# Optimization experiments

Hardware: AMD Instinct MI355X
Metric: run time of the kernel (lower is better)

Reference implementation:

```python
import jax, jax.numpy as jnp
import numpy as np

N, D = 4096, 512
TAU, ALPHA, BETA = 0.8, 0.55, 0.4
ADJ_P = 0.005  # sparse binary adjacency density (avg degree ~20)


def setup_inputs() -> dict:
    key = jax.random.key(0)
    ks = jax.random.split(key, 8)
    z1 = jax.random.normal(ks[0], (N, D), dtype=jnp.float32)
    z2 = jax.random.normal(ks[1], (N, D), dtype=jnp.float32)

    def adj(k):
        a = jax.random.bernoulli(k, ADJ_P, (N, N)).astype(jnp.float32)
        # adjacency masks are binary {0,1}; zero the diagonal like the model does
        return a * (1.0 - jnp.eye(N, dtype=jnp.float32))

    return {
        "z1": z1,
        "z2": z2,
        "adj_c": adj(ks[2]),
        "adj_m": adj(ks[3]),
        "adj_f": adj(ks[4]),
        "adj_c_aug": adj(ks[5]),
        "adj_m_aug": adj(ks[6]),
        "adj_f_aug": adj(ks[7]),
    }


def _normalize(z):
    # F.normalize(z, dim=1): divide by L2 norm clamped at 1e-12
    n = jnp.maximum(jnp.linalg.norm(z, axis=1, keepdims=True), 1e-12)
    return z / n


def _cl_loss(z, z_aug, adj, tau):
    zn = _normalize(z)
    zan = _normalize(z_aug)
    intra = jnp.exp((zn @ zn.T) / tau)          # [N, N]
    inter = jnp.exp((zn @ zan.T) / tau)         # [N, N]
    intra_diag = jnp.diagonal(intra)
    positive = jnp.diagonal(inter) + (intra * adj).sum(1) + (inter * adj).sum(1)
    denom = intra.sum(1) + inter.sum(1) - intra_diag
    adj_count = adj.sum(1) * 2.0 + 1.0
    loss = jnp.log(positive / denom) / adj_count
    return -jnp.mean(loss)


def _final_cl_loss(z, z_aug, adj, adj_aug, tau):
    return ALPHA * _cl_loss(z, z_aug, adj, tau) + BETA * _cl_loss(z_aug, z, adj_aug, tau)


def reference(z1, z2, adj_c, adj_m, adj_f, adj_c_aug, adj_m_aug, adj_f_aug):
    loss_coarse = _final_cl_loss(z1, z2, adj_c, adj_c_aug, TAU)
    loss_medium = _final_cl_loss(z1, z2, adj_m, adj_m_aug, TAU)
    loss_fine = _final_cl_loss(z1, z2, adj_f, adj_f_aug, TAU)
    loss_cross_cf = _final_cl_loss(z1, z2, adj_c, adj_f_aug, TAU * 0.8)
    loss_cross_mf = _final_cl_loss(z1, z2, adj_m, adj_f_aug, TAU * 0.9)

    sc, sm, sf = adj_c.sum(), adj_m.sum(), adj_f.sum()
    total_info = sc + sm + sf + 1e-08
    scale_loss = (sc / total_info) * loss_coarse + (sm / total_info) * loss_medium + (sf / total_info) * loss_fine
    cross_loss = 0.2 * (loss_cross_cf + loss_cross_mf)
    return scale_loss + cross_loss
```

## Files before the change

### kernel.cpp

```cpp
#include <hip/hip_runtime.h>
#include <hip/hip_bf16.h>

#define NR 4096
#define DD 512
#define CAP 64

typedef __bf16 bf16x8 __attribute__((ext_vector_type(8)));
typedef float f32x4 __attribute__((ext_vector_type(4)));
typedef unsigned short u16;

#define AS_GLOBAL(p) ((const __attribute__((address_space(1))) unsigned int*)(p))
#define AS_LDS(p)    ((__attribute__((address_space(3))) unsigned int*)(p))

__device__ __forceinline__ u16 f2bf(float x) {
    __hip_bfloat16 h = __float2bfloat16(x);
    return *reinterpret_cast<u16*>(&h);
}

__device__ __forceinline__ float blo(unsigned u) { return __uint_as_float(u << 16); }
__device__ __forceinline__ float bhi(unsigned u) { return __uint_as_float(u & 0xffff0000u); }

__global__ void norm_kernel(const float* z1, const float* z2,
                            u16* zn1, u16* zn2, float* d12) {
    const int row = blockIdx.x;
    const int t = threadIdx.x;
    const float* r1 = z1 + (size_t)row * DD;
    const float* r2 = z2 + (size_t)row * DD;
    float a0 = r1[t], a1 = r1[t + 256];
    float b0 = r2[t], b1 = r2[t + 256];
    float ss1 = a0 * a0 + a1 * a1;
    float ss2 = b0 * b0 + b1 * b1;
    #pragma unroll
    for (int m = 1; m < 64; m <<= 1) {
        ss1 += __shfl_xor(ss1, m);
        ss2 += __shfl_xor(ss2, m);
    }
    __shared__ float s1s[4], s2s[4], ds[4];
    const int wid = t >> 6, lane = t & 63;
    if (lane == 0) { s1s[wid] = ss1; s2s[wid] = ss2; }
    __syncthreads();
    const float n1 = s1s[0] + s1s[1] + s1s[2] + s1s[3];
    const float n2 = s2s[0] + s2s[1] + s2s[2] + s2s[3];
    const float inv1 = 1.0f / fmaxf(sqrtf(n1), 1e-12f);
    const float inv2 = 1.0f / fmaxf(sqrtf(n2), 1e-12f);
    const float u0 = a0 * inv1, u1 = a1 * inv1;
    const float v0 = b0 * inv2, v1 = b1 * inv2;
    zn1[(size_t)row * DD + t]       = f2bf(u0);
    zn1[(size_t)row * DD + t + 256] = f2bf(u1);
    zn2[(size_t)row * DD + t]       = f2bf(v0);
    zn2[(size_t)row * DD + t + 256] = f2bf(v1);
    float dp = u0 * v0 + u1 * v1;
    #pragma unroll
    for (int m = 1; m < 64; m <<= 1) dp += __shfl_xor(dp, m);
    if (lane == 0) ds[wid] = dp;
    __syncthreads();
    if (t == 0) d12[row] = ds[0] + ds[1] + ds[2] + ds[3];
}

__global__ __launch_bounds__(256, 3)
void fused_kernel(const u16* __restrict__ zn1, const u16* __restrict__ zn2,
                  const float* __restrict__ m0, const float* __restrict__ m1,
                  const float* __restrict__ m2, const float* __restrict__ m3,
                  const float* __restrict__ m4, const float* __restrict__ m5,
                  float* __restrict__ part, float* __restrict__ ms,
                  float* __restrict__ asum) {
    __shared__ u16 As[128 * 64];
    __shared__ u16 Bs[128 * 64];

    const int bid = blockIdx.x;
    const int tid = threadIdx.x;
    const int lane = tid & 63;

    const float C0 = 1.8033688011112042f;
    const float C1 = 2.2542110013890054f;
    const float C2 = 2.0037431123457825f;

    const int g5 = bid / 5;
    const int r5 = bid - g5 * 5;

    if (r5 < 2) {
        const int id = g5 * 2 + r5;
        int mode, by, bx;
        if (id < 1024) {
            mode = 1; by = id >> 5; bx = id & 31;
        } else {
            int k = id - 1024;
            mode = 0;
            if (k >= 528) { k -= 528; mode = 2; }
            int v = (int)((65.0f - sqrtf(4225.0f - 8.0f * (float)k)) * 0.5f);
            if (v < 0) v = 0; if (v > 31) v = 31;
            while (v < 31 && (v + 1) * 32 - ((v + 1) * v) / 2 <= k) v++;
            while (v > 0 && v * 32 - (v * (v - 1)) / 2 > k) v--;
            by = v;
            bx = by + (k - (by * 32 - (by * (by - 1)) / 2));
        }
        const int Ib = by * 128, Jb = bx * 128;
        const u16* Ag = (mode == 2) ? zn2 : zn1;
        const u16* Bg = (mode == 0) ? zn1 : zn2;
        const int p_row = mode;
        const int p_col = (mode == 1) ? 3 : mode;
        const bool do_cols = (mode == 1) || (bx != by);

        const int wid = tid >> 6;
        const int wm = wid >> 1, wn = wid & 1;
        const int quad = lane >> 4, lcol = lane & 15;

        f32x4 acc[4][4];
        #pragma unroll
        for (int a = 0; a < 4; a++)
            #pragma unroll
            for (int b = 0; b < 4; b++)
                acc[a][b] = (f32x4){0.f, 0.f, 0.f, 0.f};

        unsigned oA[4], oB[4];
        #pragma unroll
        for (int cc = 0; cc < 4; cc++) {
            const int ch = cc * 4 + wid;
            const int p = ch * 64 + lane;
            const int r = p >> 3;
            const int kb = (p & 7) ^ (r & 7);
            oA[cc] = (unsigned)((Ib + r) * DD + kb * 8);
            oB[cc] = (unsigned)((Jb + r) * DD + kb * 8);
        }

        for (int k0 = 0; k0 < DD; k0 += 64) {
            __syncthreads();
            #pragma unroll
            for (int cc = 0; cc < 4; cc++) {
                const unsigned lo = (unsigned)(cc * 4 + wid) * 1024u;
                __builtin_amdgcn_global_load_lds(AS_GLOBAL(Ag + oA[cc] + k0),
                                                 AS_LDS((char*)As + lo), 16, 0, 0);
                __builtin_amdgcn_global_load_lds(AS_GLOBAL(Bg + oB[cc] + k0),
                                                 AS_LDS((char*)Bs + lo), 16, 0, 0);
            }
            __syncthreads();
            #pragma unroll
            for (int kk = 0; kk < 64; kk += 32) {
                const int kbb = (kk >> 3) + quad;
                bf16x8 a[4], b[4];
                #pragma unroll
                for (int i = 0; i < 4; i++) {
                    const int ra = wm * 64 + i * 16 + lcol;
                    const int rb = wn * 64 + i * 16 + lcol;
                    a[i] = *(const bf16x8*)&As[ra * 64 + ((kbb ^ (ra & 7)) * 8)];
                    b[i] = *(const bf16x8*)&Bs[rb * 64 + ((kbb ^ (rb & 7)) * 8)];
                }
                #pragma unroll
                for (int mi = 0; mi < 4; mi++)
                    #pragma unroll
                    for (int ni = 0; ni < 4; ni++)
                        acc[mi][ni] = __builtin_amdgcn_mfma_f32_16x16x32_bf16(a[mi], b[ni], acc[mi][ni], 0, 0, 0);
            }
        }

        __syncthreads();
        float* eb = (float*)As;
        float* sRow = eb;
        float* sCol = eb + 768;

        float colacc[3][4];
        #pragma unroll
        for (int t = 0; t < 3; t++)
            #pragma unroll
            for (int ni = 0; ni < 4; ni++) colacc[t][ni] = 0.f;

        #pragma unroll
        for (int mi = 0; mi < 4; mi++) {
            #pragma unroll
            for (int reg = 0; reg < 4; reg++) {
                float p0 = 0.f, p1 = 0.f, p2 = 0.f;
                #pragma unroll
                for (int ni = 0; ni < 4; ni++) {
                    const float s = acc[mi][ni][reg];
                    const float e0 = __builtin_amdgcn_exp2f(s * C0);
                    const float e1 = __builtin_amdgcn_exp2f(s * C1);
                    const float e2 = __builtin_amdgcn_exp2f(s * C2);
                    p0 += e0; p1 += e1; p2 += e2;
                    colacc[0][ni] += e0; colacc[1][ni] += e1; colacc[2][ni] += e2;
                }
                #pragma unroll
                for (int msk = 1; msk < 16; msk <<= 1) {
                    p0 += __shfl_xor(p0, msk);
                    p1 += __shfl_xor(p1, msk);
                    p2 += __shfl_xor(p2, msk);
                }
                if (lcol == 0) {
                    const int r = wm * 64 + mi * 16 + quad * 4 + reg;
                    sRow[wn * 384 + 0 * 128 + r] = p0;
                    sRow[wn * 384 + 1 * 128 + r] = p1;
                    sRow[wn * 384 + 2 * 128 + r] = p2;
                }
            }
        }
        #pragma unroll
        for (int t = 0; t < 3; t++) {
            #pragma unroll
            for (int ni = 0; ni < 4; ni++) {
                float v = colacc[t][ni];
                v += __shfl_xor(v, 16); v += __shfl_xor(v, 32);
                if (quad == 0) sCol[wm * 384 + t * 128 + wn * 64 + ni * 16 + lcol] = v;
            }
        }
        __syncthreads();
        if (tid < 128) {
            const int i = Ib + tid;
            #pragma unroll
            for (int t = 0; t < 3; t++) {
                const float v = sRow[t * 128 + tid] + sRow[384 + t * 128 + tid];
                part[(((size_t)p_row * 3 + t) * 32 + bx) * NR + i] = v;
            }
        } else if (do_cols) {
            const int c = tid - 128;
            const int j = Jb + c;
            #pragma unroll
            for (int t = 0; t < 3; t++) {
                const float v = sCol[t * 128 + c] + sCol[384 + t * 128 + c];
                part[(((size_t)p_col * 3 + t) * 32 + by) * NR + j] = v;
            }
        }
    } else {
        const int sid = g5 * 3 + (r5 - 2);
        if (sid >= 3072) return;
        const int widx = tid >> 6;
        const int grp = lane >> 4;
        const int l = lane & 15;
        const int wbase = sid * 8 + widx * 2;
        const int m = wbase >> 12;
        const int i0 = wbase & (NR - 1);

        const float* M = (m == 0) ? m0 : (m == 1) ? m1 : (m == 2) ? m2
                       : (m == 3) ? m3 : (m == 4) ? m4 : m5;
        const float4* p0 = (const float4*)(M + (size_t)i0 * NR) + lane;
        const float4* p1 = (const float4*)(M + (size_t)(i0 + 1) * NR) + lane;
        unsigned long long mask0 = 0ull, mask1 = 0ull;
        #pragma unroll
        for (int t = 0; t < 16; t++) {
            const float4 va = p0[t * 64];
            const float4 vb = p1[t * 64];
            mask0 |= (unsigned long long)((va.x != 0.f ? 1u : 0u)
                   | (va.y != 0.f ? 2u : 0u)
                   | (va.z != 0.f ? 4u : 0u)
                   | (va.w != 0.f ? 8u : 0u)) << (t * 4);
            mask1 |= (unsigned long long)((vb.x != 0.f ? 1u : 0u)
                   | (vb.y != 0.f ? 2u : 0u)
                   | (vb.z != 0.f ? 4u : 0u)
                   | (vb.w != 0.f ? 8u : 0u)) << (t * 4);
        }
        const int n0 = __popcll(mask0), n1 = __popcll(mask1);
        int off0 = n0, off1 = n1;
        #pragma unroll
        for (int d = 1; d < 64; d <<= 1) {
            const int t0 = __shfl_up(off0, d);
            const int t1 = __shfl_up(off1, d);
            if (lane >= d) { off0 += t0; off1 += t1; }
        }
        const int total0 = __shfl(off0, 63), total1 = __shfl(off1, 63);
        int* lidx0 = ((int*)As) + widx * 128;
        int* lidx1 = lidx0 + 64;
        int pos = off0 - n0;
        unsigned long long mm = mask0;
        while (mm) {
            const int b = __ffsll(mm) - 1;
            mm &= mm - 1;
            if (pos < CAP) lidx0[pos] = ((b >> 2) * 64 + lane) * 4 + (b & 3);
            pos++;
        }
        pos = off1 - n1;
        mm = mask1;
        while (mm) {
            const int b = __ffsll(mm) - 1;
            mm &= mm - 1;
            if (pos < CAP) lidx1[pos] = ((b >> 2) * 64 + lane) * 4 + (b & 3);
            pos++;
        }
        if (lane == 63) {
            asum[(size_t)m * NR + i0]     = (float)total0;
            asum[(size_t)m * NR + i0 + 1] = (float)total1;
        }
        const int cnt0 = min(total0, CAP), cnt1 = min(total1, CAP);
        const int jreg0 = lidx0[lane];
        const int jreg1 = lidx1[lane];

        int nslot; int slot[3]; float coef[3];
        switch (m) {
            case 0: nslot = 2; slot[0] = 0; coef[0] = C0; slot[1] = 3; coef[1] = C1; break;
            case 1: nslot = 2; slot[0] = 1; coef[0] = C0; slot[1] = 4; coef[1] = C2; break;
            case 2: nslot = 1; slot[0] = 2; coef[0] = C0; break;
            case 3: nslot = 1; slot[0] = 0; coef[0] = C0; break;
            case 4: nslot = 1; slot[0] = 1; coef[0] = C0; break;
            default: nslot = 3; slot[0] = 2; coef[0] = C0; slot[1] = 3; coef[1] = C1;
                     slot[2] = 4; coef[2] = C2; break;
        }

        const u16* A = (m < 3) ? zn1 : zn2;

        for (int rr = 0; rr < 2; rr++) {
            const int i = i0 + rr;
            const int cnt = rr ? cnt1 : cnt0;
            const int jreg = rr ? jreg1 : jreg0;

            unsigned au[16];
            {
                const uint4* ap = (const uint4*)(A + (size_t)i * DD) + l * 4;
                #pragma unroll
                for (int t = 0; t < 4; t++) {
                    const uint4 r = ap[t];
                    au[t * 4 + 0] = r.x; au[t * 4 + 1] = r.y;
                    au[t * 4 + 2] = r.z; au[t * 4 + 3] = r.w;
                }
            }

            float acc[3][2] = {{0.f, 0.f}, {0.f, 0.f}, {0.f, 0.f}};

            for (int q0 = 0; q0 < cnt; q0 += 4) {
                const int q = q0 + grp;
                const bool valid = q < cnt;
                const int j = __shfl(jreg, valid ? q : 0);

                const uint4* pj1 = (const uint4*)(zn1 + (size_t)j * DD) + l * 4;
                const uint4* pj2 = (const uint4*)(zn2 + (size_t)j * DD) + l * 4;
                uint4 r1[4], r2[4];
                #pragma unroll
                for (int t = 0; t < 4; t++) { r1[t] = pj1[t]; r2[t] = pj2[t]; }

                float s10 = 0.f, s11 = 0.f, s20 = 0.f, s21 = 0.f;
                #pragma unroll
                for (int t = 0; t < 4; t++) {
                    const unsigned* u1 = (const unsigned*)&r1[t];
                    const unsigned* u2 = (const unsigned*)&r2[t];
                    #pragma unroll
                    for (int qd = 0; qd < 4; qd++) {
                        const unsigned aw = au[t * 4 + qd];
                        const float alo = blo(aw), ahi = bhi(aw);
                        s10 += alo * blo(u1[qd]); s11 += ahi * bhi(u1[qd]);
                        s20 += alo * blo(u2[qd]); s21 += ahi * bhi(u2[qd]);
                    }
                }
                float d1 = s10 + s11, d2 = s20 + s21;
                #pragma unroll
                for (int msk = 1; msk < 16; msk <<= 1) {
                    d1 += __shfl_xor(d1, msk);
                    d2 += __shfl_xor(d2, msk);
                }
                const float e1 = (m < 3) ? d1 : d2;
                const float e2 = (m < 3) ? d2 : d1;
                if (valid) {
                    for (int s = 0; s < nslot; s++) {
                        acc[s][0] += __builtin_amdgcn_exp2f(e1 * coef[s]);
                        acc[s][1] += __builtin_amdgcn_exp2f(e2 * coef[s]);
                    }
                }
            }

            #pragma unroll
            for (int s = 0; s < 3; s++) {
                #pragma unroll
                for (int h = 0; h < 2; h++) {
                    float v = acc[s][h];
                    v += __shfl_xor(v, 16);
                    v += __shfl_xor(v, 32);
                    acc[s][h] = v;
                }
            }
            if (lane == 0) {
                const int pb = (m < 3) ? 0 : 2;
                for (int s = 0; s < nslot; s++) {
                    ms[((pb)     * 5 + slot[s]) * NR + i] = acc[s][0];
                    ms[((pb + 1) * 5 + slot[s]) * NR + i] = acc[s][1];
                }
            }
        }
    }
}

__global__ __launch_bounds__(256)
void reduce_kernel(const float* __restrict__ part, float* __restrict__ rs) {
    const int g = blockIdx.x * 256 + threadIdx.x;
    const int pt = g >> 12;
    const int i = g & (NR - 1);
    const float* base = part + ((size_t)pt * 32) * NR + i;
    float s = 0.f;
    #pragma unroll
    for (int k = 0; k < 32; k++) s += base[(size_t)k * NR];
    rs[(size_t)pt * NR + i] = s;
}

__global__ void finalize_kernel(const float* rs, const float* ms, const float* asum,
                                const float* d12, float* out) {
    const int t = threadIdx.x;
    const int tA[5] = {0, 0, 0, 1, 2};
    const int kA[5] = {0, 1, 2, 3, 4};
    const int aA[5] = {0, 1, 2, 0, 1};
    const int aB[5] = {3, 4, 5, 5, 5};
    const float it[3] = {1.25f, 1.5625f, 1.3888888888888888f};
    const float e1t[3] = {expf(1.25f), expf(1.5625f), expf(1.3888888888888888f)};

    float LA[5] = {0, 0, 0, 0, 0}, LB[5] = {0, 0, 0, 0, 0};
    float sc = 0.f, sm = 0.f, sf = 0.f;

    for (int i = t; i < NR; i += 256) {
        const float d = d12[i];
        float ed[3];
        ed[0] = __expf(d * it[0]); ed[1] = __expf(d * it[1]); ed[2] = __expf(d * it[2]);
        float R[4][3], M[4][5], A6[6];
        #pragma unroll
        for (int p = 0; p < 4; p++) {
            #pragma unroll
            for (int tt = 0; tt < 3; tt++) R[p][tt] = rs[(p * 3 + tt) * NR + i];
            #pragma unroll
            for (int k = 0; k < 5; k++) M[p][k] = ms[(p * 5 + k) * NR + i];
        }
        #pragma unroll
        for (int a = 0; a < 6; a++) A6[a] = asum[a * NR + i];

        #pragma unroll
        for (int c = 0; c < 5; c++) {
            const int tt = tA[c], k = kA[c];
            float pos = ed[tt] + M[0][k] + M[1][k];
            float den = R[0][tt] + R[1][tt] - e1t[tt];
            float cnt = 2.f * A6[aA[c]] + 1.f;
            LA[c] += __logf(pos / den) / cnt;
            pos = ed[tt] + M[2][k] + M[3][k];
            den = R[2][tt] + R[3][tt] - e1t[tt];
            cnt = 2.f * A6[aB[c]] + 1.f;
            LB[c] += __logf(pos / den) / cnt;
        }
        sc += A6[0]; sm += A6[1]; sf += A6[2];
    }

    __shared__ float red[256];
    float vals[13] = {LA[0], LA[1], LA[2], LA[3], LA[4],
                      LB[0], LB[1], LB[2], LB[3], LB[4], sc, sm, sf};
    __shared__ float tot[13];
    for (int q = 0; q < 13; q++) {
        red[t] = vals[q];
        __syncthreads();
        for (int s = 128; s > 0; s >>= 1) {
            if (t < s) red[t] += red[t + s];
            __syncthreads();
        }
        if (t == 0) tot[q] = red[0];
        __syncthreads();
    }
    if (t == 0) {
        float Ac[5], Bc[5];
        #pragma unroll
        for (int c = 0; c < 5; c++) {
            Ac[c] = -tot[c] / (float)NR;
            Bc[c] = -tot[5 + c] / (float)NR;
        }
        const float ALPHA = 0.55f, BETA = 0.4f;
        const float Lc  = ALPHA * Ac[0] + BETA * Bc[0];
        const float Lm  = ALPHA * Ac[1] + BETA * Bc[1];
        const float Lf  = ALPHA * Ac[2] + BETA * Bc[2];
        const float Lcf = ALPHA * Ac[3] + BETA * Bc[3];
        const float Lmf = ALPHA * Ac[4] + BETA * Bc[4];
        const float scs = tot[10], sms = tot[11], sfs = tot[12];
        const float tot_info = scs + sms + sfs + 1e-8f;
        out[0] = (scs * Lc + sms * Lm + sfs * Lf) / tot_info + 0.2f * (Lcf + Lmf);
    }
}

extern "C" void kernel_launch(void* const* d_in, const int* in_sizes, int n_in,
                              void* d_out, int out_size, void* d_ws, size_t ws_size,
                              hipStream_t stream) {
    const float* z1  = (const float*)d_in[0];
    const float* z2  = (const float*)d_in[1];
    const float* ac  = (const float*)d_in[2];
    const float* am  = (const float*)d_in[3];
    const float* af  = (const float*)d_in[4];
    const float* aca = (const float*)d_in[5];
    const float* ama = (const float*)d_in[6];
    const float* afa = (const float*)d_in[7];

    float* ws   = (float*)d_ws;
    float* rs   = ws;
    float* ms   = rs + 12 * NR;
    float* asum = ms + 20 * NR;
    float* d12  = asum + 6 * NR;
    u16* zn1 = (u16*)(d12 + NR);
    u16* zn2 = zn1 + (size_t)NR * DD;
    float* part = (float*)(zn2 + (size_t)NR * DD);

    norm_kernel<<<NR, 256, 0, stream>>>(z1, z2, zn1, zn2, d12);
    fused_kernel<<<5200, 256, 0, stream>>>(zn1, zn2, ac, am, af, aca, ama, afa,
                                           part, ms, asum);
    reduce_kernel<<<12 * NR / 256, 256, 0, stream>>>(part, rs);
    finalize_kernel<<<1, 256, 0, stream>>>(rs, ms, asum, d12, (float*)d_out);
}
```

Baseline: 511.7 us.

## Use 512-thread blocks with 8 waves per 128x128 similarity tile

Doubles the fused kernel's block size from 256 to 512 threads. Each 128x128 GEMM tile is now split across 8 waves in a 2x4 grid, each owning a 64x32 sub-tile, and each adjacency-mask block processes 16 rows instead of 8. The interleaving of GEMM and mask blocks and the grid size are rebalanced to match. The aim is more waves per tile and fewer accumulator registers per wave, for better latency hiding. The cost is more LDS reads per MFMA, since A fragments are reloaded by more waves, plus an extra partial-sum reduction step in the epilogue.

```diff
diff --git a/kernel.cpp b/kernel.cpp
--- a/kernel.cpp
+++ b/kernel.cpp
@@ -57,7 +57,7 @@
     if (t == 0) d12[row] = ds[0] + ds[1] + ds[2] + ds[3];
 }
 
-__global__ __launch_bounds__(256, 3)
+__global__ __launch_bounds__(512, 3)
 void fused_kernel(const u16* __restrict__ zn1, const u16* __restrict__ zn2,
                   const float* __restrict__ m0, const float* __restrict__ m1,
                   const float* __restrict__ m2, const float* __restrict__ m3,
@@ -75,11 +75,11 @@
     const float C1 = 2.2542110013890054f;
     const float C2 = 2.0037431123457825f;
 
-    const int g5 = bid / 5;
-    const int r5 = bid - g5 * 5;
-
-    if (r5 < 2) {
-        const int id = g5 * 2 + r5;
+    const int g7 = bid / 7;
+    const int r7 = bid - g7 * 7;
+
+    if (r7 < 4) {
+        const int id = g7 * 4 + r7;
         int mode, by, bx;
         if (id < 1024) {
             mode = 1; by = id >> 5; bx = id & 31;
@@ -102,20 +102,21 @@
         const bool do_cols = (mode == 1) || (bx != by);
 
         const int wid = tid >> 6;
-        const int wm = wid >> 1, wn = wid & 1;
+        const int wm = wid >> 2;
+        const int wn = wid & 3;
         const int quad = lane >> 4, lcol = lane & 15;
 
-        f32x4 acc[4][4];
+        f32x4 acc[4][2];
         #pragma unroll
         for (int a = 0; a < 4; a++)
             #pragma unroll
-            for (int b = 0; b < 4; b++)
+            for (int b = 0; b < 2; b++)
                 acc[a][b] = (f32x4){0.f, 0.f, 0.f, 0.f};
 
-        unsigned oA[4], oB[4];
-        #pragma unroll
-        for (int cc = 0; cc < 4; cc++) {
-            const int ch = cc * 4 + wid;
+        unsigned oA[2], oB[2];
+        #pragma unroll
+        for (int cc = 0; cc < 2; cc++) {
+            const int ch = cc * 8 + wid;
             const int p = ch * 64 + lane;
             const int r = p >> 3;
             const int kb = (p & 7) ^ (r & 7);
@@ -126,8 +127,8 @@
         for (int k0 = 0; k0 < DD; k0 += 64) {
             __syncthreads();
             #pragma unroll
-            for (int cc = 0; cc < 4; cc++) {
-                const unsigned lo = (unsigned)(cc * 4 + wid) * 1024u;
+            for (int cc = 0; cc < 2; cc++) {
+                const unsigned lo = (unsigned)(cc * 8 + wid) * 1024u;
                 __builtin_amdgcn_global_load_lds(AS_GLOBAL(Ag + oA[cc] + k0),
                                                  AS_LDS((char*)As + lo), 16, 0, 0);
                 __builtin_amdgcn_global_load_lds(AS_GLOBAL(Bg + oB[cc] + k0),
@@ -137,18 +138,21 @@
             #pragma unroll
             for (int kk = 0; kk < 64; kk += 32) {
                 const int kbb = (kk >> 3) + quad;
-                bf16x8 a[4], b[4];
+                bf16x8 a[4], b[2];
                 #pragma unroll
                 for (int i = 0; i < 4; i++) {
                     const int ra = wm * 64 + i * 16 + lcol;
-                    const int rb = wn * 64 + i * 16 + lcol;
                     a[i] = *(const bf16x8*)&As[ra * 64 + ((kbb ^ (ra & 7)) * 8)];
+                }
+                #pragma unroll
+                for (int i = 0; i < 2; i++) {
+                    const int rb = wn * 32 + i * 16 + lcol;
                     b[i] = *(const bf16x8*)&Bs[rb * 64 + ((kbb ^ (rb & 7)) * 8)];
                 }
                 #pragma unroll
                 for (int mi = 0; mi < 4; mi++)
                     #pragma unroll
-                    for (int ni = 0; ni < 4; ni++)
+                    for (int ni = 0; ni < 2; ni++)
                         acc[mi][ni] = __builtin_amdgcn_mfma_f32_16x16x32_bf16(a[mi], b[ni], acc[mi][ni], 0, 0, 0);
             }
         }
@@ -156,13 +160,13 @@
         __syncthreads();
         float* eb = (float*)As;
         float* sRow = eb;
-        float* sCol = eb + 768;
-
-        float colacc[3][4];
+        float* sCol = eb + 1536;
+
+        float colacc[3][2];
         #pragma unroll
         for (int t = 0; t < 3; t++)
             #pragma unroll
-            for (int ni = 0; ni < 4; ni++) colacc[t][ni] = 0.f;
+            for (int ni = 0; ni < 2; ni++) colacc[t][ni] = 0.f;
 
         #pragma unroll
         for (int mi = 0; mi < 4; mi++) {
@@ -170,7 +174,7 @@
             for (int reg = 0; reg < 4; reg++) {
                 float p0 = 0.f, p1 = 0.f, p2 = 0.f;
                 #pragma unroll
-                for (int ni = 0; ni < 4; ni++) {
+                for (int ni = 0; ni < 2; ni++) {
                     const float s = acc[mi][ni][reg];
                     const float e0 = __builtin_amdgcn_exp2f(s * C0);
                     const float e1 = __builtin_amdgcn_exp2f(s * C1);
@@ -186,19 +190,19 @@
                 }
                 if (lcol == 0) {
                     const int r = wm * 64 + mi * 16 + quad * 4 + reg;
-                    sRow[wn * 384 + 0 * 128 + r] = p0;
-                    sRow[wn * 384 + 1 * 128 + r] = p1;
-                    sRow[wn * 384 + 2 * 128 + r] = p2;
+                    sRow[(wn * 3 + 0) * 128 + r] = p0;
+                    sRow[(wn * 3 + 1) * 128 + r] = p1;
+                    sRow[(wn * 3 + 2) * 128 + r] = p2;
                 }
             }
         }
         #pragma unroll
         for (int t = 0; t < 3; t++) {
             #pragma unroll
-            for (int ni = 0; ni < 4; ni++) {
+            for (int ni = 0; ni < 2; ni++) {
                 float v = colacc[t][ni];
                 v += __shfl_xor(v, 16); v += __shfl_xor(v, 32);
-                if (quad == 0) sCol[wm * 384 + t * 128 + wn * 64 + ni * 16 + lcol] = v;
+                if (quad == 0) sCol[(wm * 3 + t) * 128 + wn * 32 + ni * 16 + lcol] = v;
             }
         }
         __syncthreads();
@@ -206,25 +210,26 @@
             const int i = Ib + tid;
             #pragma unroll
             for (int t = 0; t < 3; t++) {
-                const float v = sRow[t * 128 + tid] + sRow[384 + t * 128 + tid];
+                const float v = sRow[(0 * 3 + t) * 128 + tid] + sRow[(1 * 3 + t) * 128 + tid]
+                              + sRow[(2 * 3 + t) * 128 + tid] + sRow[(3 * 3 + t) * 128 + tid];
                 part[(((size_t)p_row * 3 + t) * 32 + bx) * NR + i] = v;
             }
-        } else if (do_cols) {
+        } else if (tid < 256 && do_cols) {
             const int c = tid - 128;
             const int j = Jb + c;
             #pragma unroll
             for (int t = 0; t < 3; t++) {
-                const float v = sCol[t * 128 + c] + sCol[384 + t * 128 + c];
+                const float v = sCol[(0 * 3 + t) * 128 + c] + sCol[(1 * 3 + t) * 128 + c];
                 part[(((size_t)p_col * 3 + t) * 32 + by) * NR + j] = v;
             }
         }
     } else {
-        const int sid = g5 * 3 + (r5 - 2);
-        if (sid >= 3072) return;
+        const int sid = g7 * 3 + (r7 - 4);
+        if (sid >= 1536) return;
         const int widx = tid >> 6;
         const int grp = lane >> 4;
         const int l = lane & 15;
-        const int wbase = sid * 8 + widx * 2;
+        const int wbase = sid * 16 + widx * 2;
         const int m = wbase >> 12;
         const int i0 = wbase & (NR - 1);
 
@@ -483,7 +488,7 @@
     float* part = (float*)(zn2 + (size_t)NR * DD);
 
     norm_kernel<<<NR, 256, 0, stream>>>(z1, z2, zn1, zn2, d12);
-    fused_kernel<<<5200, 256, 0, stream>>>(zn1, zn2, ac, am, af, aca, ama, afa,
+    fused_kernel<<<3640, 512, 0, stream>>>(zn1, zn2, ac, am, af, aca, ama, afa,
                                            part, ms, asum);
     reduce_kernel<<<12 * NR / 256, 256, 0, stream>>>(part, rs);
     finalize_kernel<<<1, 256, 0, stream>>>(rs, ms, asum, d12, (float*)d_out);
```

Result: no change. 506.5 us (-1.0%).
